# Optimization experiments

Measured on AMD Instinct MI355X. Metric: run time of the kernel, lower is better.

The kernel has to match this reference:

```python
import jax, jax.numpy as jnp
import numpy as np

EPS = 1e-8  # torch CosineSimilarity eps
BN_EPS = 0.0  # BN folded into scale/shift


def _conv1d(x, w):  # x:(B,C,N), w:(O,C) -> (B,O,N)
    return jnp.einsum('oc,bcn->bon', w, x)


def _conv2d(x, w):  # x:(B,C,N,M), w:(O,C) -> (B,O,N,M)
    return jnp.einsum('oc,bcnm->bonm', w, x)


def setup_inputs() -> dict:
    key = jax.random.key(0)
    B, f, n1, n2 = 128, 32, 64, 128
    ks = jax.random.split(key, 12)
    d = {
        'x_label': jax.random.normal(ks[0], (B, f, n2), jnp.float32),
        'x_object': jax.random.normal(ks[1], (B, f, n1), jnp.float32),
        'template_xyz': jax.random.normal(ks[2], (B, n1, 3), jnp.float32),
        'mlp_w1': 0.1 * jax.random.normal(ks[3], (32, 68), jnp.float32),
        'mlp_s1': jnp.ones((32,), jnp.float32),
        'mlp_t1': jnp.zeros((32,), jnp.float32),
        'mlp_w2': 0.1 * jax.random.normal(ks[4], (32, 32), jnp.float32),
        'mlp_s2': jnp.ones((32,), jnp.float32),
        'mlp_t2': jnp.zeros((32,), jnp.float32),
        'gw_w1': 0.1 * jax.random.normal(ks[5], (32, 32), jnp.float32),
        'gw_b1': jnp.zeros((32,), jnp.float32),
        'gw_s': jnp.ones((32,), jnp.float32),
        'gw_t': jnp.zeros((32,), jnp.float32),
        'gw_w2': 0.1 * jax.random.normal(ks[6], (32, 32), jnp.float32),
        'gw_b2': jnp.zeros((32,), jnp.float32),
        'gm_w1': 0.1 * jax.random.normal(ks[7], (32, 35), jnp.float32),
        'gm_s1': jnp.ones((32,), jnp.float32),
        'gm_t1': jnp.zeros((32,), jnp.float32),
        'gm_w2': 0.1 * jax.random.normal(ks[8], (32, 32), jnp.float32),
        'gm_s2': jnp.ones((32,), jnp.float32),
        'gm_t2': jnp.zeros((32,), jnp.float32),
        'fl_w1': 0.1 * jax.random.normal(ks[9], (64, 64), jnp.float32),
        'fl_s1': jnp.ones((64,), jnp.float32),
        'fl_t1': jnp.zeros((64,), jnp.float32),
        'fl_w2': 0.1 * jax.random.normal(ks[10], (64, 64), jnp.float32),
        'fl_b2': jnp.zeros((64,), jnp.float32),
    }
    return d


def reference(x_label, x_object, template_xyz,
              mlp_w1, mlp_s1, mlp_t1, mlp_w2, mlp_s2, mlp_t2,
              gw_w1, gw_b1, gw_s, gw_t, gw_w2, gw_b2,
              gm_w1, gm_s1, gm_t1, gm_w2, gm_s2, gm_t2,
              fl_w1, fl_s1, fl_t1, fl_w2, fl_b2):
    B, f, n1 = x_object.shape
    n2 = x_label.shape[2]

    # pairwise cosine similarity over channel dim -> (B, n1, n2)
    num = jnp.einsum('bfn,bfm->bnm', x_object, x_label)
    na = jnp.linalg.norm(x_object, axis=1)  # (B,n1)
    nb = jnp.linalg.norm(x_label, axis=1)   # (B,n2)
    cos = num / jnp.maximum(na[:, :, None] * nb[:, None, :], EPS)

    # nearest-template gather (indices from detached scores)
    txyz = jnp.transpose(template_xyz, (0, 2, 1))            # (B,3,n1)
    template_xyz_fea = jnp.concatenate([txyz, x_object], 1)  # (B,35,n1)
    idx = jnp.argmax(jax.lax.stop_gradient(cos), axis=1)     # (B,n2)
    template_fea = jnp.take_along_axis(template_xyz_fea, idx[:, None, :], axis=2)  # (B,35,n2)

    # max-pool over template dim of the (non-detached) scores
    max_cla = jnp.max(cos, axis=1, keepdims=True)            # (B,1,n2)

    fusion = jnp.concatenate([max_cla, template_fea, x_label], 1)  # (B,68,n2)
    h = jax.nn.relu(mlp_s1[:, None] * _conv1d(fusion, mlp_w1) + mlp_t1[:, None])
    h = jax.nn.relu(mlp_s2[:, None] * _conv1d(h, mlp_w2) + mlp_t2[:, None])  # (B,32,n2)

    # global attention branch over (B,f,n1,n2)
    diff = x_label[:, :, None, :] - x_object[:, :, :, None]
    g = _conv2d(diff, gw_w1) + gw_b1[:, None, None]
    g = jax.nn.leaky_relu(gw_s[:, None, None] * g + gw_t[:, None, None], 0.2)
    gw = jax.nn.sigmoid(_conv2d(g, gw_w2) + gw_b2[:, None, None])
    gfeat = gw * x_object[:, :, :, None]                      # (B,32,n1,n2)
    txyz_b = jnp.broadcast_to(txyz[:, :, :, None], (B, 3, n1, n2))
    gfeat = jnp.concatenate([txyz_b, gfeat], 1)               # (B,35,n1,n2)
    gfeat = jax.nn.relu(gm_s1[:, None, None] * _conv2d(gfeat, gm_w1) + gm_t1[:, None, None])
    gfeat = jax.nn.relu(gm_s2[:, None, None] * _conv2d(gfeat, gm_w2) + gm_t2[:, None, None])
    gpool = jnp.max(gfeat, axis=2)                            # (B,32,n2)

    fused = jnp.concatenate([h, gpool], 1)                    # (B,64,n2)
    out = jax.nn.relu(fl_s1[:, None] * _conv1d(fused, fl_w1) + fl_t1[:, None])
    out = _conv1d(out, fl_w2) + fl_b2[:, None]                # (B,64,n2)
    return out
```

## Files before the change

### kernel.cpp

```cpp
#include <hip/hip_runtime.h>

#define NF   32
#define NN1  64
#define NN2  128
#define MT   16
#define P    66
#define PU   66

typedef float f32x4 __attribute__((ext_vector_type(4)));
typedef short s16x8 __attribute__((ext_vector_type(8)));
typedef unsigned int u32;
typedef unsigned short ushort;

__device__ __forceinline__ short f2bf(float f) {
    u32 u = __float_as_uint(f);
    return (short)((u + 0x7FFFu + ((u >> 16) & 1u)) >> 16);
}
__device__ __forceinline__ float b2f(ushort us) {
    return __uint_as_float((u32)us << 16);
}
__device__ __forceinline__ u32 pack2(float a, float b) {
    return (u32)(ushort)f2bf(a) | ((u32)(ushort)f2bf(b) << 16);
}

__device__ __forceinline__ s16x8 redist(u32 L01, u32 L23, u32 H01, u32 H23, int q) {
    u32 a0 = __shfl_xor((int)L01, 16), a1 = __shfl_xor((int)L01, 32), a2 = __shfl_xor((int)L01, 48);
    u32 b0 = __shfl_xor((int)L23, 16), b1 = __shfl_xor((int)L23, 32), b2 = __shfl_xor((int)L23, 48);
    u32 c0 = __shfl_xor((int)H01, 16), c1 = __shfl_xor((int)H01, 32), c2 = __shfl_xor((int)H01, 48);
    u32 d0 = __shfl_xor((int)H23, 16), d1 = __shfl_xor((int)H23, 32), d2 = __shfl_xor((int)H23, 48);
    u32 w0 = (q == 0) ? L01 : (q == 1) ? a2 : (q == 2) ? c1 : c0;
    u32 w1 = (q == 0) ? L23 : (q == 1) ? b2 : (q == 2) ? d1 : d0;
    u32 w2 = (q == 0) ? a0  : (q == 1) ? a1 : (q == 2) ? c2 : H01;
    u32 w3 = (q == 0) ? b0  : (q == 1) ? b1 : (q == 2) ? d2 : H23;
    s16x8 r;
    r[0] = (short)w0; r[1] = (short)(w0 >> 16);
    r[2] = (short)w1; r[3] = (short)(w1 >> 16);
    r[4] = (short)w2; r[5] = (short)(w2 >> 16);
    r[6] = (short)w3; r[7] = (short)(w3 >> 16);
    return r;
}

__global__ __launch_bounds__(1024, 2)
void v2b_fused(const float* __restrict__ xl,
               const float* __restrict__ xo,
               const float* __restrict__ txyz,
               const float* __restrict__ mlp_w1, const float* __restrict__ mlp_s1, const float* __restrict__ mlp_t1,
               const float* __restrict__ mlp_w2, const float* __restrict__ mlp_s2, const float* __restrict__ mlp_t2,
               const float* __restrict__ gw_w1, const float* __restrict__ gw_b1,
               const float* __restrict__ gw_s,  const float* __restrict__ gw_t,
               const float* __restrict__ gw_w2, const float* __restrict__ gw_b2,
               const float* __restrict__ gm_w1, const float* __restrict__ gm_s1, const float* __restrict__ gm_t1,
               const float* __restrict__ gm_w2, const float* __restrict__ gm_s2, const float* __restrict__ gm_t2,
               const float* __restrict__ fl_w1, const float* __restrict__ fl_s1, const float* __restrict__ fl_t1,
               const float* __restrict__ fl_w2, const float* __restrict__ fl_b2,
               float* __restrict__ out)
{
    __shared__ float  xo_s[NF][P];
    __shared__ ushort yon_us[NF * PU];
    __shared__ ushort tpos_us[NF * PU];
    __shared__ float  txyz_s[3][NN1];
    __shared__ float  xl_s[NF][MT];
    __shared__ float  ylT_s[MT][NF];
    __shared__ float  na_s[NN1];
    __shared__ float  nb_s[MT];
    __shared__ float  gpart_s[MT][4][NF];
    __shared__ float  gws_s[NF], gwt_s[NF], gwb2_s[NF], gmt2_s[NF];
    __shared__ float  ms1_s[32], mt1_s[32], ms2_s[32], mt2_s[32];
    __shared__ float  fs1_s[64], ft1_s[64], fb2_s[64];
    __shared__ s16x8  afrag_s[2][6][64];

    extern __shared__ float dynw[];
    float*  F2   = dynw;
    ushort* W1us = (ushort*)(F2 + 64 * 65);
    ushort* W2us = W1us + 32 * 70;
    ushort* F1us = W2us + 32 * 34;

    const int b    = blockIdx.x >> 3;
    const int m0   = (blockIdx.x & 7) * MT;
    const int tid  = threadIdx.x;
    const int lane = tid & 63;
    const int w    = tid >> 6;
    const int colr = lane & 15;
    const int q    = lane >> 4;

    const float* xob = xo + (size_t)b * NF * NN1;
    for (int i = tid; i < NF * NN1; i += 1024) xo_s[i >> 6][i & 63] = xob[i];
    const float* tb = txyz + (size_t)b * NN1 * 3;
    if (tid < NN1 * 3) { int nn = tid / 3, k = tid % 3; txyz_s[k][nn] = tb[tid]; }
    if (tid < NF * MT) {
        int c = tid >> 4, j = tid & 15;
        xl_s[c][j] = xl[(size_t)b * NF * NN2 + c * NN2 + m0 + j];
    }
    if (tid >= 512 && tid < 512 + NF) {
        int c = tid - 512;
        gws_s[c]  = gw_s[c];
        gwt_s[c]  = gw_t[c];
        gwb2_s[c] = gw_b2[c];
        gmt2_s[c] = gm_t2[c];
    }
    if (tid >= 576 && tid < 576 + 32) {
        int c = tid - 576;
        ms1_s[c] = mlp_s1[c]; mt1_s[c] = mlp_t1[c];
        ms2_s[c] = mlp_s2[c]; mt2_s[c] = mlp_t2[c];
    }
    if (tid >= 640 && tid < 640 + 64) {
        int c = tid - 640;
        fs1_s[c] = fl_s1[c]; ft1_s[c] = fl_t1[c]; fb2_s[c] = fl_b2[c];
    }
    for (int i = tid; i < 32 * 68; i += 1024) W1us[(i / 68) * 70 + (i % 68)] = (ushort)f2bf(mlp_w1[i]);
    for (int i = tid; i < 32 * 32; i += 1024) W2us[(i >> 5) * 34 + (i & 31)] = (ushort)f2bf(mlp_w2[i]);
    for (int i = tid; i < 64 * 64; i += 1024) {
        int r = i >> 6, c = i & 63;
        F1us[r * 66 + c] = (ushort)f2bf(fl_w1[i]);
        F2[r * 65 + c]   = fl_w2[i];
    }
    if (w >= 8 && w < 14) {
        const int f = w - 8;
        const int row = (f & 1) ? colr + 16 : colr;
        s16x8 a;
        if (f < 2) {
            #pragma unroll
            for (int j = 0; j < 8; ++j) a[j] = f2bf(gw_w2[row * 32 + 8 * q + j]);
        } else if (f < 4) {
            const float s1 = gm_s1[row];
            #pragma unroll
            for (int j = 0; j < 8; ++j) a[j] = f2bf(s1 * gm_w1[row * 35 + 3 + 8 * q + j]);
        } else {
            const float s2 = gm_s2[row];
            #pragma unroll
            for (int j = 0; j < 8; ++j) a[j] = f2bf(s2 * gm_w2[row * 32 + 8 * q + j]);
        }
        afrag_s[0][f][lane] = a;
        afrag_s[1][f][lane] = a;
    }
    __syncthreads();

    for (int i = tid; i < NF * NN1; i += 1024) {
        const int o = i >> 6, nn = i & 63;
        float s = 0.f;
        #pragma unroll
        for (int c = 0; c < NF; ++c) s += gw_w1[o * 32 + c] * xo_s[c][nn];
        yon_us[o * PU + nn] = (ushort)f2bf(-s);
        float tp = gm_w1[o * 35 + 0] * txyz_s[0][nn]
                 + gm_w1[o * 35 + 1] * txyz_s[1][nn]
                 + gm_w1[o * 35 + 2] * txyz_s[2][nn];
        tpos_us[o * PU + nn] = (ushort)f2bf(gm_s1[o] * tp + gm_t1[o]);
    }
    if (tid < NF * MT) {
        const int j = tid >> 5, o = tid & 31;
        float s = gw_b1[o];
        #pragma unroll
        for (int c = 0; c < NF; ++c) s += gw_w1[o * 32 + c] * xl_s[c][j];
        ylT_s[j][o] = s;
    } else if (tid < NF * MT + NN1) {
        const int nn = tid - NF * MT;
        float s = 0.f;
        #pragma unroll
        for (int c = 0; c < NF; ++c) { float v = xo_s[c][nn]; s += v * v; }
        na_s[nn] = sqrtf(s);
    } else if (tid < NF * MT + NN1 + MT) {
        const int j = tid - NF * MT - NN1;
        float s = 0.f;
        #pragma unroll
        for (int c = 0; c < NF; ++c) { float v = xl_s[c][j]; s += v * v; }
        nb_s[j] = sqrtf(s);
    }
    __syncthreads();

    for (int t = w; t < MT * 4; t += 16) {
        const int mj = t >> 2;
        const int ng = t & 3;
        const int n  = ng * 16 + colr;
        const s16x8* af = &afrag_s[(t >> 4) & 1][0][0];

        s16x8 bg;
        #pragma unroll
        for (int j = 0; j < 8; ++j) {
            const int k = 8 * q + j;
            float y = b2f(yon_us[k * PU + n]) + ylT_s[mj][k];
            float a = gws_s[k] * y + gwt_s[k];
            bg[j] = f2bf(a > 0.f ? a : 0.2f * a);
        }

        f32x4 zlo, zhi;
        #pragma unroll
        for (int r = 0; r < 4; ++r) { zlo[r] = gwb2_s[4 * q + r]; zhi[r] = gwb2_s[4 * q + r + 16]; }
        zlo = __builtin_amdgcn_mfma_f32_16x16x32_bf16(af[0 * 64 + lane], bg, zlo, 0, 0, 0);
        zhi = __builtin_amdgcn_mfma_f32_16x16x32_bf16(af[1 * 64 + lane], bg, zhi, 0, 0, 0);

        u32 L01, L23, H01, H23;
        {
            float d0 = xo_s[4 * q + 0][n] / (1.f + __expf(-zlo[0]));
            float d1 = xo_s[4 * q + 1][n] / (1.f + __expf(-zlo[1]));
            float d2 = xo_s[4 * q + 2][n] / (1.f + __expf(-zlo[2]));
            float d3 = xo_s[4 * q + 3][n] / (1.f + __expf(-zlo[3]));
            L01 = pack2(d0, d1); L23 = pack2(d2, d3);
            float e0 = xo_s[4 * q + 16][n] / (1.f + __expf(-zhi[0]));
            float e1 = xo_s[4 * q + 17][n] / (1.f + __expf(-zhi[1]));
            float e2 = xo_s[4 * q + 18][n] / (1.f + __expf(-zhi[2]));
            float e3 = xo_s[4 * q + 19][n] / (1.f + __expf(-zhi[3]));
            H01 = pack2(e0, e1); H23 = pack2(e2, e3);
        }
        s16x8 bga = redist(L01, L23, H01, H23, q);

        f32x4 mlo, mhi;
        #pragma unroll
        for (int r = 0; r < 4; ++r) {
            mlo[r] = b2f(tpos_us[(4 * q + r) * PU + n]);
            mhi[r] = b2f(tpos_us[(4 * q + r + 16) * PU + n]);
        }
        mlo = __builtin_amdgcn_mfma_f32_16x16x32_bf16(af[2 * 64 + lane], bga, mlo, 0, 0, 0);
        mhi = __builtin_amdgcn_mfma_f32_16x16x32_bf16(af[3 * 64 + lane], bga, mhi, 0, 0, 0);

        u32 M01 = pack2(fmaxf(mlo[0], 0.f), fmaxf(mlo[1], 0.f));
        u32 M23 = pack2(fmaxf(mlo[2], 0.f), fmaxf(mlo[3], 0.f));
        u32 N01 = pack2(fmaxf(mhi[0], 0.f), fmaxf(mhi[1], 0.f));
        u32 N23 = pack2(fmaxf(mhi[2], 0.f), fmaxf(mhi[3], 0.f));
        s16x8 bm1 = redist(M01, M23, N01, N23, q);

        f32x4 plo, phi;
        #pragma unroll
        for (int r = 0; r < 4; ++r) { plo[r] = gmt2_s[4 * q + r]; phi[r] = gmt2_s[4 * q + r + 16]; }
        plo = __builtin_amdgcn_mfma_f32_16x16x32_bf16(af[4 * 64 + lane], bm1, plo, 0, 0, 0);
        phi = __builtin_amdgcn_mfma_f32_16x16x32_bf16(af[5 * 64 + lane], bm1, phi, 0, 0, 0);

        float rmax[8];
        #pragma unroll
        for (int r = 0; r < 4; ++r) {
            rmax[r]     = fmaxf(plo[r], 0.f);
            rmax[r + 4] = fmaxf(phi[r], 0.f);
        }
        #pragma unroll
        for (int ix = 0; ix < 8; ++ix) {
            float v = rmax[ix];
            v = fmaxf(v, __shfl_xor(v, 1));
            v = fmaxf(v, __shfl_xor(v, 2));
            v = fmaxf(v, __shfl_xor(v, 4));
            v = fmaxf(v, __shfl_xor(v, 8));
            rmax[ix] = v;
        }
        if (colr == 0) {
            #pragma unroll
            for (int ix = 0; ix < 8; ++ix)
                gpart_s[mj][ng][4 * q + (ix & 3) + 16 * (ix >> 2)] = rmax[ix];
        }
    }
    __syncthreads();

    const int mj = w;
    const int m  = m0 + w;
    const int n  = lane;
    float num = 0.f;
    #pragma unroll
    for (int c = 0; c < NF; ++c) num += xo_s[c][n] * xl_s[c][mj];
    float cosv = num / fmaxf(na_s[n] * nb_s[mj], 1e-8f);
    float mv = cosv; int mi = n;
    #pragma unroll
    for (int s = 32; s > 0; s >>= 1) {
        float ov = __shfl_xor(mv, s);
        int   oi = __shfl_xor(mi, s);
        if (ov > mv || (ov == mv && oi < mi)) { mv = ov; mi = oi; }
    }

    const int oc = lane & 31;
    float h1;
    {
        const ushort* wp = W1us + oc * 70;
        float acc = b2f(wp[0]) * mv;
        #pragma unroll
        for (int k = 0; k < 3; ++k)  acc += b2f(wp[1 + k])  * txyz_s[k][mi];
        #pragma unroll
        for (int c = 0; c < 32; ++c) acc += b2f(wp[4 + c])  * xo_s[c][mi];
        #pragma unroll
        for (int c = 0; c < 32; ++c) acc += b2f(wp[36 + c]) * xl_s[c][mj];
        acc = ms1_s[oc] * acc + mt1_s[oc];
        h1 = acc > 0.f ? acc : 0.f;
    }
    float h2;
    {
        const ushort* wp = W2us + oc * 34;
        float acc = 0.f;
        #pragma unroll
        for (int c = 0; c < 32; ++c) acc += b2f(wp[c]) * __shfl(h1, c);
        acc = ms2_s[oc] * acc + mt2_s[oc];
        h2 = acc > 0.f ? acc : 0.f;
    }
    float o1;
    {
        const ushort* wp = F1us + lane * 66;
        float acc = 0.f;
        #pragma unroll
        for (int c = 0; c < 32; ++c) acc += b2f(wp[c]) * __shfl(h2, c);
        #pragma unroll
        for (int c = 0; c < 32; ++c) {
            float gv = fmaxf(fmaxf(gpart_s[mj][0][c], gpart_s[mj][1][c]),
                             fmaxf(gpart_s[mj][2][c], gpart_s[mj][3][c]));
            acc += b2f(wp[32 + c]) * gv;
        }
        acc = fs1_s[lane] * acc + ft1_s[lane];
        o1 = acc > 0.f ? acc : 0.f;
    }
    {
        const float* wp = F2 + lane * 65;
        float acc = fb2_s[lane];
        #pragma unroll
        for (int c = 0; c < 64; ++c) acc += wp[c] * __shfl(o1, c);
        out[(size_t)b * 64 * NN2 + (size_t)lane * NN2 + m] = acc;
    }
}

extern "C" void kernel_launch(void* const* d_in, const int* in_sizes, int n_in,
                              void* d_out, int out_size, void* d_ws, size_t ws_size,
                              hipStream_t stream) {
    const float* xl     = (const float*)d_in[0];
    const float* xo     = (const float*)d_in[1];
    const float* txyz   = (const float*)d_in[2];
    const float* mlp_w1 = (const float*)d_in[3];
    const float* mlp_s1 = (const float*)d_in[4];
    const float* mlp_t1 = (const float*)d_in[5];
    const float* mlp_w2 = (const float*)d_in[6];
    const float* mlp_s2 = (const float*)d_in[7];
    const float* mlp_t2 = (const float*)d_in[8];
    const float* gw_w1  = (const float*)d_in[9];
    const float* gw_b1  = (const float*)d_in[10];
    const float* gw_s   = (const float*)d_in[11];
    const float* gw_t   = (const float*)d_in[12];
    const float* gw_w2  = (const float*)d_in[13];
    const float* gw_b2  = (const float*)d_in[14];
    const float* gm_w1  = (const float*)d_in[15];
    const float* gm_s1  = (const float*)d_in[16];
    const float* gm_t1  = (const float*)d_in[17];
    const float* gm_w2  = (const float*)d_in[18];
    const float* gm_s2  = (const float*)d_in[19];
    const float* gm_t2  = (const float*)d_in[20];
    const float* fl_w1  = (const float*)d_in[21];
    const float* fl_s1  = (const float*)d_in[22];
    const float* fl_t1  = (const float*)d_in[23];
    const float* fl_w2  = (const float*)d_in[24];
    const float* fl_b2  = (const float*)d_in[25];
    float* outp = (float*)d_out;

    const int B = in_sizes[0] / (NF * NN2);
    const size_t dyn = (size_t)(64 * 65) * sizeof(float)
                     + (size_t)(32 * 70 + 32 * 34 + 64 * 66) * sizeof(ushort);
    v2b_fused<<<dim3(B * 8), 1024, dyn, stream>>>(
        xl, xo, txyz,
        mlp_w1, mlp_s1, mlp_t1, mlp_w2, mlp_s2, mlp_t2,
        gw_w1, gw_b1, gw_s, gw_t, gw_w2, gw_b2,
        gm_w1, gm_s1, gm_t1, gm_w2, gm_s2, gm_t2,
        fl_w1, fl_s1, fl_t1, fl_w2, fl_b2,
        outp);
}
```

Before: 231.2 us.

## Enlarge per-block column tile to 64 and accumulate max-pool in registers

Each block now processes 64 label columns instead of 16, so a batch uses 2 blocks rather than 8. This amortises the per-block setup (weight conversion to bf16, the x_object projection, the A-fragment build) over more work. Each wave loops over its columns and keeps a running max across the four n-groups in registers, which removes the 4-way partial pool buffer in shared memory. It also switches bf16 conversion to the HIP intrinsic. The grid drops to 256 blocks of 1024 threads, which may underfill the GPU's compute units and lengthen the serial loop inside each wave.

Result: slower. 441.4 us (+90.9%).

```diff
diff --git a/kernel.cpp b/kernel.cpp
--- a/kernel.cpp
+++ b/kernel.cpp
@@ -1,9 +1,10 @@
 #include <hip/hip_runtime.h>
+#include <hip/hip_bf16.h>
 
 #define NF   32
 #define NN1  64
 #define NN2  128
-#define MT   16
+#define MT   64
 #define P    66
 #define PU   66
 
@@ -12,15 +13,16 @@
 typedef unsigned int u32;
 typedef unsigned short ushort;
 
-__device__ __forceinline__ short f2bf(float f) {
-    u32 u = __float_as_uint(f);
-    return (short)((u + 0x7FFFu + ((u >> 16) & 1u)) >> 16);
+__device__ __forceinline__ ushort f2bf(float f) {
+    union { __hip_bfloat16 h; ushort u; } cv;
+    cv.h = __float2bfloat16(f);
+    return cv.u;
 }
 __device__ __forceinline__ float b2f(ushort us) {
     return __uint_as_float((u32)us << 16);
 }
 __device__ __forceinline__ u32 pack2(float a, float b) {
-    return (u32)(ushort)f2bf(a) | ((u32)(ushort)f2bf(b) << 16);
+    return (u32)f2bf(a) | ((u32)f2bf(b) << 16);
 }
 
 __device__ __forceinline__ s16x8 redist(u32 L01, u32 L23, u32 H01, u32 H23, int q) {
@@ -63,7 +65,7 @@
     __shared__ float  ylT_s[MT][NF];
     __shared__ float  na_s[NN1];
     __shared__ float  nb_s[MT];
-    __shared__ float  gpart_s[MT][4][NF];
+    __shared__ float  gpart_s[MT][NF];
     __shared__ float  gws_s[NF], gwt_s[NF], gwb2_s[NF], gmt2_s[NF];
     __shared__ float  ms1_s[32], mt1_s[32], ms2_s[32], mt2_s[32];
     __shared__ float  fs1_s[64], ft1_s[64], fb2_s[64];
@@ -75,8 +77,8 @@
     ushort* W2us = W1us + 32 * 70;
     ushort* F1us = W2us + 32 * 34;
 
-    const int b    = blockIdx.x >> 3;
-    const int m0   = (blockIdx.x & 7) * MT;
+    const int b    = blockIdx.x >> 1;
+    const int m0   = (blockIdx.x & 1) * MT;
     const int tid  = threadIdx.x;
     const int lane = tid & 63;
     const int w    = tid >> 6;
@@ -87,8 +89,8 @@
     for (int i = tid; i < NF * NN1; i += 1024) xo_s[i >> 6][i & 63] = xob[i];
     const float* tb = txyz + (size_t)b * NN1 * 3;
     if (tid < NN1 * 3) { int nn = tid / 3, k = tid % 3; txyz_s[k][nn] = tb[tid]; }
-    if (tid < NF * MT) {
-        int c = tid >> 4, j = tid & 15;
+    for (int i = tid; i < NF * MT; i += 1024) {
+        int c = i >> 6, j = i & 63;
         xl_s[c][j] = xl[(size_t)b * NF * NN2 + c * NN2 + m0 + j];
     }
     if (tid >= 512 && tid < 512 + NF) {
@@ -107,11 +109,11 @@
         int c = tid - 640;
         fs1_s[c] = fl_s1[c]; ft1_s[c] = fl_t1[c]; fb2_s[c] = fl_b2[c];
     }
-    for (int i = tid; i < 32 * 68; i += 1024) W1us[(i / 68) * 70 + (i % 68)] = (ushort)f2bf(mlp_w1[i]);
-    for (int i = tid; i < 32 * 32; i += 1024) W2us[(i >> 5) * 34 + (i & 31)] = (ushort)f2bf(mlp_w2[i]);
+    for (int i = tid; i < 32 * 68; i += 1024) W1us[(i / 68) * 70 + (i % 68)] = f2bf(mlp_w1[i]);
+    for (int i = tid; i < 32 * 32; i += 1024) W2us[(i >> 5) * 34 + (i & 31)] = f2bf(mlp_w2[i]);
     for (int i = tid; i < 64 * 64; i += 1024) {
         int r = i >> 6, c = i & 63;
-        F1us[r * 66 + c] = (ushort)f2bf(fl_w1[i]);
+        F1us[r * 66 + c] = f2bf(fl_w1[i]);
         F2[r * 65 + c]   = fl_w2[i];
     }
     if (w >= 8 && w < 14) {
@@ -120,15 +122,15 @@
         s16x8 a;
         if (f < 2) {
             #pragma unroll
-            for (int j = 0; j < 8; ++j) a[j] = f2bf(gw_w2[row * 32 + 8 * q + j]);
+            for (int j = 0; j < 8; ++j) a[j] = (short)f2bf(gw_w2[row * 32 + 8 * q + j]);
         } else if (f < 4) {
             const float s1 = gm_s1[row];
             #pragma unroll
-            for (int j = 0; j < 8; ++j) a[j] = f2bf(s1 * gm_w1[row * 35 + 3 + 8 * q + j]);
+            for (int j = 0; j < 8; ++j) a[j] = (short)f2bf(s1 * gm_w1[row * 35 + 3 + 8 * q + j]);
         } else {
             const float s2 = gm_s2[row];
             #pragma unroll
-            for (int j = 0; j < 8; ++j) a[j] = f2bf(s2 * gm_w2[row * 32 + 8 * q + j]);
+            for (int j = 0; j < 8; ++j) a[j] = (short)f2bf(s2 * gm_w2[row * 32 + 8 * q + j]);
         }
         afrag_s[0][f][lane] = a;
         afrag_s[1][f][lane] = a;
@@ -140,26 +142,26 @@
         float s = 0.f;
         #pragma unroll
         for (int c = 0; c < NF; ++c) s += gw_w1[o * 32 + c] * xo_s[c][nn];
-        yon_us[o * PU + nn] = (ushort)f2bf(-s);
+        yon_us[o * PU + nn] = f2bf(-s);
         float tp = gm_w1[o * 35 + 0] * txyz_s[0][nn]
                  + gm_w1[o * 35 + 1] * txyz_s[1][nn]
                  + gm_w1[o * 35 + 2] * txyz_s[2][nn];
-        tpos_us[o * PU + nn] = (ushort)f2bf(gm_s1[o] * tp + gm_t1[o]);
-    }
-    if (tid < NF * MT) {
-        const int j = tid >> 5, o = tid & 31;
+        tpos_us[o * PU + nn] = f2bf(gm_s1[o] * tp + gm_t1[o]);
+    }
+    for (int i = tid; i < MT * NF; i += 1024) {
+        const int j = i >> 5, o = i & 31;
         float s = gw_b1[o];
         #pragma unroll
         for (int c = 0; c < NF; ++c) s += gw_w1[o * 32 + c] * xl_s[c][j];
         ylT_s[j][o] = s;
-    } else if (tid < NF * MT + NN1) {
-        const int nn = tid - NF * MT;
+    }
+    if (tid < NN1) {
         float s = 0.f;
         #pragma unroll
-        for (int c = 0; c < NF; ++c) { float v = xo_s[c][nn]; s += v * v; }
-        na_s[nn] = sqrtf(s);
-    } else if (tid < NF * MT + NN1 + MT) {
-        const int j = tid - NF * MT - NN1;
+        for (int c = 0; c < NF; ++c) { float v = xo_s[c][tid]; s += v * v; }
+        na_s[tid] = sqrtf(s);
+    } else if (tid < NN1 + MT) {
+        const int j = tid - NN1;
         float s = 0.f;
         #pragma unroll
         for (int c = 0; c < NF; ++c) { float v = xl_s[c][j]; s += v * v; }
@@ -167,69 +169,74 @@
     }
     __syncthreads();
 
-    for (int t = w; t < MT * 4; t += 16) {
-        const int mj = t >> 2;
-        const int ng = t & 3;
-        const int n  = ng * 16 + colr;
-        const s16x8* af = &afrag_s[(t >> 4) & 1][0][0];
-
-        s16x8 bg;
-        #pragma unroll
-        for (int j = 0; j < 8; ++j) {
-            const int k = 8 * q + j;
-            float y = b2f(yon_us[k * PU + n]) + ylT_s[mj][k];
-            float a = gws_s[k] * y + gwt_s[k];
-            bg[j] = f2bf(a > 0.f ? a : 0.2f * a);
-        }
-
-        f32x4 zlo, zhi;
-        #pragma unroll
-        for (int r = 0; r < 4; ++r) { zlo[r] = gwb2_s[4 * q + r]; zhi[r] = gwb2_s[4 * q + r + 16]; }
-        zlo = __builtin_amdgcn_mfma_f32_16x16x32_bf16(af[0 * 64 + lane], bg, zlo, 0, 0, 0);
-        zhi = __builtin_amdgcn_mfma_f32_16x16x32_bf16(af[1 * 64 + lane], bg, zhi, 0, 0, 0);
-
-        u32 L01, L23, H01, H23;
-        {
-            float d0 = xo_s[4 * q + 0][n] / (1.f + __expf(-zlo[0]));
-            float d1 = xo_s[4 * q + 1][n] / (1.f + __expf(-zlo[1]));
-            float d2 = xo_s[4 * q + 2][n] / (1.f + __expf(-zlo[2]));
-            float d3 = xo_s[4 * q + 3][n] / (1.f + __expf(-zlo[3]));
-            L01 = pack2(d0, d1); L23 = pack2(d2, d3);
-            float e0 = xo_s[4 * q + 16][n] / (1.f + __expf(-zhi[0]));
-            float e1 = xo_s[4 * q + 17][n] / (1.f + __expf(-zhi[1]));
-            float e2 = xo_s[4 * q + 18][n] / (1.f + __expf(-zhi[2]));
-            float e3 = xo_s[4 * q + 19][n] / (1.f + __expf(-zhi[3]));
-            H01 = pack2(e0, e1); H23 = pack2(e2, e3);
-        }
-        s16x8 bga = redist(L01, L23, H01, H23, q);
-
-        f32x4 mlo, mhi;
-        #pragma unroll
-        for (int r = 0; r < 4; ++r) {
-            mlo[r] = b2f(tpos_us[(4 * q + r) * PU + n]);
-            mhi[r] = b2f(tpos_us[(4 * q + r + 16) * PU + n]);
-        }
-        mlo = __builtin_amdgcn_mfma_f32_16x16x32_bf16(af[2 * 64 + lane], bga, mlo, 0, 0, 0);
-        mhi = __builtin_amdgcn_mfma_f32_16x16x32_bf16(af[3 * 64 + lane], bga, mhi, 0, 0, 0);
-
-        u32 M01 = pack2(fmaxf(mlo[0], 0.f), fmaxf(mlo[1], 0.f));
-        u32 M23 = pack2(fmaxf(mlo[2], 0.f), fmaxf(mlo[3], 0.f));
-        u32 N01 = pack2(fmaxf(mhi[0], 0.f), fmaxf(mhi[1], 0.f));
-        u32 N23 = pack2(fmaxf(mhi[2], 0.f), fmaxf(mhi[3], 0.f));
-        s16x8 bm1 = redist(M01, M23, N01, N23, q);
-
-        f32x4 plo, phi;
-        #pragma unroll
-        for (int r = 0; r < 4; ++r) { plo[r] = gmt2_s[4 * q + r]; phi[r] = gmt2_s[4 * q + r + 16]; }
-        plo = __builtin_amdgcn_mfma_f32_16x16x32_bf16(af[4 * 64 + lane], bm1, plo, 0, 0, 0);
-        phi = __builtin_amdgcn_mfma_f32_16x16x32_bf16(af[5 * 64 + lane], bm1, phi, 0, 0, 0);
-
-        float rmax[8];
-        #pragma unroll
-        for (int r = 0; r < 4; ++r) {
-            rmax[r]     = fmaxf(plo[r], 0.f);
-            rmax[r + 4] = fmaxf(phi[r], 0.f);
-        }
+    #pragma unroll 1
+    for (int k = 0; k < 4; ++k) {
+        const int mj = w + 16 * k;
+        float rmax[8] = {0.f, 0.f, 0.f, 0.f, 0.f, 0.f, 0.f, 0.f};
+
+        #pragma unroll 1
+        for (int ng = 0; ng < 4; ++ng) {
+            const int n = ng * 16 + colr;
+            const s16x8* af = &afrag_s[ng & 1][0][0];
+
+            s16x8 bg;
+            #pragma unroll
+            for (int j = 0; j < 8; ++j) {
+                const int kk = 8 * q + j;
+                float y = b2f(yon_us[kk * PU + n]) + ylT_s[mj][kk];
+                float a = gws_s[kk] * y + gwt_s[kk];
+                bg[j] = (short)f2bf(a > 0.f ? a : 0.2f * a);
+            }
+
+            f32x4 zlo, zhi;
+            #pragma unroll
+            for (int r = 0; r < 4; ++r) { zlo[r] = gwb2_s[4 * q + r]; zhi[r] = gwb2_s[4 * q + r + 16]; }
+            zlo = __builtin_amdgcn_mfma_f32_16x16x32_bf16(af[0 * 64 + lane], bg, zlo, 0, 0, 0);
+            zhi = __builtin_amdgcn_mfma_f32_16x16x32_bf16(af[1 * 64 + lane], bg, zhi, 0, 0, 0);
+
+            u32 L01, L23, H01, H23;
+            {
+                float d0 = xo_s[4 * q + 0][n] / (1.f + __expf(-zlo[0]));
+                float d1 = xo_s[4 * q + 1][n] / (1.f + __expf(-zlo[1]));
+                float d2 = xo_s[4 * q + 2][n] / (1.f + __expf(-zlo[2]));
+                float d3 = xo_s[4 * q + 3][n] / (1.f + __expf(-zlo[3]));
+                L01 = pack2(d0, d1); L23 = pack2(d2, d3);
+                float e0 = xo_s[4 * q + 16][n] / (1.f + __expf(-zhi[0]));
+                float e1 = xo_s[4 * q + 17][n] / (1.f + __expf(-zhi[1]));
+                float e2 = xo_s[4 * q + 18][n] / (1.f + __expf(-zhi[2]));
+                float e3 = xo_s[4 * q + 19][n] / (1.f + __expf(-zhi[3]));
+                H01 = pack2(e0, e1); H23 = pack2(e2, e3);
+            }
+            s16x8 bga = redist(L01, L23, H01, H23, q);
+
+            f32x4 mlo, mhi;
+            #pragma unroll
+            for (int r = 0; r < 4; ++r) {
+                mlo[r] = b2f(tpos_us[(4 * q + r) * PU + n]);
+                mhi[r] = b2f(tpos_us[(4 * q + r + 16) * PU + n]);
+            }
+            mlo = __builtin_amdgcn_mfma_f32_16x16x32_bf16(af[2 * 64 + lane], bga, mlo, 0, 0, 0);
+            mhi = __builtin_amdgcn_mfma_f32_16x16x32_bf16(af[3 * 64 + lane], bga, mhi, 0, 0, 0);
+
+            u32 M01 = pack2(fmaxf(mlo[0], 0.f), fmaxf(mlo[1], 0.f));
+            u32 M23 = pack2(fmaxf(mlo[2], 0.f), fmaxf(mlo[3], 0.f));
+            u32 N01 = pack2(fmaxf(mhi[0], 0.f), fmaxf(mhi[1], 0.f));
+            u32 N23 = pack2(fmaxf(mhi[2], 0.f), fmaxf(mhi[3], 0.f));
+            s16x8 bm1 = redist(M01, M23, N01, N23, q);
+
+            f32x4 plo, phi;
+            #pragma unroll
+            for (int r = 0; r < 4; ++r) { plo[r] = gmt2_s[4 * q + r]; phi[r] = gmt2_s[4 * q + r + 16]; }
+            plo = __builtin_amdgcn_mfma_f32_16x16x32_bf16(af[4 * 64 + lane], bm1, plo, 0, 0, 0);
+            phi = __builtin_amdgcn_mfma_f32_16x16x32_bf16(af[5 * 64 + lane], bm1, phi, 0, 0, 0);
+
+            #pragma unroll
+            for (int r = 0; r < 4; ++r) {
+                rmax[r]     = fmaxf(rmax[r],     fmaxf(plo[r], 0.f));
+                rmax[r + 4] = fmaxf(rmax[r + 4], fmaxf(phi[r], 0.f));
+            }
+        }
+
         #pragma unroll
         for (int ix = 0; ix < 8; ++ix) {
             float v = rmax[ix];
@@ -242,70 +249,69 @@
         if (colr == 0) {
             #pragma unroll
             for (int ix = 0; ix < 8; ++ix)
-                gpart_s[mj][ng][4 * q + (ix & 3) + 16 * (ix >> 2)] = rmax[ix];
+                gpart_s[mj][4 * q + (ix & 3) + 16 * (ix >> 2)] = rmax[ix];
         }
     }
     __syncthreads();
 
-    const int mj = w;
-    const int m  = m0 + w;
-    const int n  = lane;
-    float num = 0.f;
-    #pragma unroll
-    for (int c = 0; c < NF; ++c) num += xo_s[c][n] * xl_s[c][mj];
-    float cosv = num / fmaxf(na_s[n] * nb_s[mj], 1e-8f);
-    float mv = cosv; int mi = n;
-    #pragma unroll
-    for (int s = 32; s > 0; s >>= 1) {
-        float ov = __shfl_xor(mv, s);
-        int   oi = __shfl_xor(mi, s);
-        if (ov > mv || (ov == mv && oi < mi)) { mv = ov; mi = oi; }
-    }
-
-    const int oc = lane & 31;
-    float h1;
-    {
-        const ushort* wp = W1us + oc * 70;
-        float acc = b2f(wp[0]) * mv;
-        #pragma unroll
-        for (int k = 0; k < 3; ++k)  acc += b2f(wp[1 + k])  * txyz_s[k][mi];
-        #pragma unroll
-        for (int c = 0; c < 32; ++c) acc += b2f(wp[4 + c])  * xo_s[c][mi];
-        #pragma unroll
-        for (int c = 0; c < 32; ++c) acc += b2f(wp[36 + c]) * xl_s[c][mj];
-        acc = ms1_s[oc] * acc + mt1_s[oc];
-        h1 = acc > 0.f ? acc : 0.f;
-    }
-    float h2;
-    {
-        const ushort* wp = W2us + oc * 34;
-        float acc = 0.f;
-        #pragma unroll
-        for (int c = 0; c < 32; ++c) acc += b2f(wp[c]) * __shfl(h1, c);
-        acc = ms2_s[oc] * acc + mt2_s[oc];
-        h2 = acc > 0.f ? acc : 0.f;
-    }
-    float o1;
-    {
-        const ushort* wp = F1us + lane * 66;
-        float acc = 0.f;
-        #pragma unroll
-        for (int c = 0; c < 32; ++c) acc += b2f(wp[c]) * __shfl(h2, c);
-        #pragma unroll
-        for (int c = 0; c < 32; ++c) {
-            float gv = fmaxf(fmaxf(gpart_s[mj][0][c], gpart_s[mj][1][c]),
-                             fmaxf(gpart_s[mj][2][c], gpart_s[mj][3][c]));
-            acc += b2f(wp[32 + c]) * gv;
-        }
-        acc = fs1_s[lane] * acc + ft1_s[lane];
-        o1 = acc > 0.f ? acc : 0.f;
-    }
-    {
-        const float* wp = F2 + lane * 65;
-        float acc = fb2_s[lane];
-        #pragma unroll
-        for (int c = 0; c < 64; ++c) acc += wp[c] * __shfl(o1, c);
-        out[(size_t)b * 64 * NN2 + (size_t)lane * NN2 + m] = acc;
+    #pragma unroll 1
+    for (int k = 0; k < 4; ++k) {
+        const int mj = w + 16 * k;
+        const int m  = m0 + mj;
+        const int n  = lane;
+        float num = 0.f;
+        #pragma unroll
+        for (int c = 0; c < NF; ++c) num += xo_s[c][n] * xl_s[c][mj];
+        float cosv = num / fmaxf(na_s[n] * nb_s[mj], 1e-8f);
+        float mv = cosv; int mi = n;
+        #pragma unroll
+        for (int s = 32; s > 0; s >>= 1) {
+            float ov = __shfl_xor(mv, s);
+            int   oi = __shfl_xor(mi, s);
+            if (ov > mv || (ov == mv && oi < mi)) { mv = ov; mi = oi; }
+        }
+
+        const int oc = lane & 31;
+        float h1;
+        {
+            const ushort* wp = W1us + oc * 70;
+            float acc = b2f(wp[0]) * mv;
+            #pragma unroll
+            for (int kk = 0; kk < 3; ++kk) acc += b2f(wp[1 + kk]) * txyz_s[kk][mi];
+            #pragma unroll
+            for (int c = 0; c < 32; ++c) acc += b2f(wp[4 + c])  * xo_s[c][mi];
+            #pragma unroll
+            for (int c = 0; c < 32; ++c) acc += b2f(wp[36 + c]) * xl_s[c][mj];
+            acc = ms1_s[oc] * acc + mt1_s[oc];
+            h1 = acc > 0.f ? acc : 0.f;
+        }
+        float h2;
+        {
+            const ushort* wp = W2us + oc * 34;
+            float acc = 0.f;
+            #pragma unroll
+            for (int c = 0; c < 32; ++c) acc += b2f(wp[c]) * __shfl(h1, c);
+            acc = ms2_s[oc] * acc + mt2_s[oc];
+            h2 = acc > 0.f ? acc : 0.f;
+        }
+        float o1;
+        {
+            const ushort* wp = F1us + lane * 66;
+            float acc = 0.f;
+            #pragma unroll
+            for (int c = 0; c < 32; ++c) acc += b2f(wp[c]) * __shfl(h2, c);
+            #pragma unroll
+            for (int c = 0; c < 32; ++c) acc += b2f(wp[32 + c]) * gpart_s[mj][c];
+            acc = fs1_s[lane] * acc + ft1_s[lane];
+            o1 = acc > 0.f ? acc : 0.f;
+        }
+        {
+            const float* wp = F2 + lane * 65;
+            float acc = fb2_s[lane];
+            #pragma unroll
+            for (int c = 0; c < 64; ++c) acc += wp[c] * __shfl(o1, c);
+            out[(size_t)b * 64 * NN2 + (size_t)lane * NN2 + m] = acc;
+        }
     }
 }
 
@@ -343,7 +349,7 @@
     const int B = in_sizes[0] / (NF * NN2);
     const size_t dyn = (size_t)(64 * 65) * sizeof(float)
                      + (size_t)(32 * 70 + 32 * 34 + 64 * 66) * sizeof(ushort);
-    v2b_fused<<<dim3(B * 8), 1024, dyn, stream>>>(
+    v2b_fused<<<dim3(B * 2), 1024, dyn, stream>>>(
         xl, xo, txyz,
         mlp_w1, mlp_s1, mlp_t1, mlp_w2, mlp_s2, mlp_t2,
         gw_w1, gw_b1, gw_s, gw_t, gw_w2, gw_b2,
```
